# Performance work log

Hardware: AMD Instinct MI355X
Metric: run time of the kernel (lower is better)

Reference implementation:

```python
import jax, jax.numpy as jnp
import numpy as np
import math

B, T, D_MOTION = 2, 1536, 256
D_MODEL, N_HEADS, D_FF, N_LAYERS = 512, 8, 2048, 6
D_HEAD = D_MODEL // N_HEADS
FPS = 30
PERIOD = FPS // 2
CONTEXT_FRAMES = 10
NEG = -1e9  # large negative instead of -inf so fully-masked rows give uniform attn, not NaN


def _w(k, shape, fan_in):
    return jax.random.normal(k, shape, jnp.float32) / np.sqrt(fan_in)


def setup_inputs() -> dict:
    key = jax.random.key(0)
    ks = jax.random.split(key, 16)
    L = N_LAYERS
    din = D_MOTION + 5 + 1
    inp = {
        'motion': jax.random.normal(ks[0], (B, T, D_MOTION), jnp.float32),
        'traj': jax.random.normal(ks[1], (B, T, 5), jnp.float32),
        'me_w1': _w(ks[2], (din, D_MODEL), din), 'me_b1': jnp.zeros((D_MODEL,), jnp.float32),
        'me_w2': _w(ks[3], (D_MODEL, D_MODEL), D_MODEL), 'me_b2': jnp.zeros((D_MODEL,), jnp.float32),
        'wq': _w(ks[4], (L, D_MODEL, D_MODEL), D_MODEL), 'bq': jnp.zeros((L, D_MODEL), jnp.float32),
        'wk': _w(ks[5], (L, D_MODEL, D_MODEL), D_MODEL), 'bk': jnp.zeros((L, D_MODEL), jnp.float32),
        'wv': _w(ks[6], (L, D_MODEL, D_MODEL), D_MODEL), 'bv': jnp.zeros((L, D_MODEL), jnp.float32),
        'wo': _w(ks[7], (L, D_MODEL, D_MODEL), D_MODEL), 'bo': jnp.zeros((L, D_MODEL), jnp.float32),
        'ln1_g': jnp.ones((L, D_MODEL), jnp.float32), 'ln1_b': jnp.zeros((L, D_MODEL), jnp.float32),
        'ffn_w1': _w(ks[8], (L, D_MODEL, D_FF), D_MODEL), 'ffn_b1': jnp.zeros((L, D_FF), jnp.float32),
        'ffn_w2': _w(ks[9], (L, D_FF, D_MODEL), D_FF), 'ffn_b2': jnp.zeros((L, D_MODEL), jnp.float32),
        'ln2_g': jnp.ones((L, D_MODEL), jnp.float32), 'ln2_b': jnp.zeros((L, D_MODEL), jnp.float32),
        'fln_g': jnp.ones((D_MODEL,), jnp.float32), 'fln_b': jnp.zeros((D_MODEL,), jnp.float32),
        'dec_w1': _w(ks[10], (D_MODEL, D_MODEL), D_MODEL), 'dec_b1': jnp.zeros((D_MODEL,), jnp.float32),
        'dec_w2': _w(ks[11], (D_MODEL, D_MOTION), D_MODEL), 'dec_b2': jnp.zeros((D_MOTION,), jnp.float32),
    }
    return inp


def _layer_norm(x, g, b):
    m = jnp.mean(x, axis=-1, keepdims=True)
    v = jnp.mean((x - m) ** 2, axis=-1, keepdims=True)
    return (x - m) * jax.lax.rsqrt(v + 1e-5) * g + b


def _leaky(x):
    return jnp.where(x >= 0, x, 0.01 * x)


def _forward(motion, traj, me_w1, me_b1, me_w2, me_b2, wq, bq, wk, bk, wv, bv, wo, bo,
             ln1_g, ln1_b, ffn_w1, ffn_b1, ffn_w2, ffn_b2, ln2_g, ln2_b,
             fln_g, fln_b, dec_w1, dec_b1, dec_w2, dec_b2):
    idx = jnp.arange(T)
    dist = jnp.abs(idx[:, None] - idx[None, :])                       # [T,T]
    atten_bias = -(dist // PERIOD).astype(jnp.float32)                # periodic distance bias

    # context mask: keep first context_frames and last frame
    batch_mask = jnp.ones((T, 1), jnp.float32).at[CONTEXT_FRAMES:-1].set(0.0)
    mask = jnp.broadcast_to(batch_mask[None], (B, T, 1))              # [B,T,1]
    cf = jnp.ones((T,), bool).at[CONTEXT_FRAMES:-1].set(False)        # constrained frames

    original_motion = motion
    motion = motion * mask

    # motion encoder (dropout inactive at eval)
    h = jnp.concatenate([motion, traj, mask], axis=-1)                # [B,T,D_MOTION+6]
    x = _leaky(h @ me_w1 + me_b1)
    x = _leaky(x @ me_w2 + me_b2)

    # periodic positional embedding (sinusoidal on pos mod period)
    pos = jnp.mod(jnp.arange(T, dtype=jnp.float32), float(PERIOD))
    half = D_MODEL // 2
    div = jnp.exp(-np.log(10000.0) * (2.0 * jnp.arange(half, dtype=jnp.float32)) / D_MODEL)
    ang = pos[:, None] * div[None, :]
    pe = jnp.concatenate([jnp.sin(ang), jnp.cos(ang)], axis=-1)       # [T,D_MODEL]
    x = x + pe[None]

    # dynamically growing attention window
    num_trans = T - CONTEXT_FRAMES - 1
    ksz = math.ceil(num_trans / 2 / N_LAYERS) * 2 + 1
    kern = jnp.ones((ksz,), jnp.float32)
    thr = ksz // 2
    scale = 1.0 / np.sqrt(D_HEAD)

    for i in range(N_LAYERS):
        # attn mask: True = blocked
        amask = (dist > thr) | (~cf)[None, :]                         # [T,T]
        h = _layer_norm(x, ln1_g[i], ln1_b[i])                        # pre-layernorm
        q = (h @ wq[i] + bq[i]).reshape(B, T, N_HEADS, D_HEAD)
        k = (h @ wk[i] + bk[i]).reshape(B, T, N_HEADS, D_HEAD)
        v = (h @ wv[i] + bv[i]).reshape(B, T, N_HEADS, D_HEAD)
        scores = jnp.einsum('bqhd,bkhd->bhqk', q, k) * scale + atten_bias
        scores = jnp.where(amask[None, None], NEG, scores)
        attn = jax.nn.softmax(scores, axis=-1)
        out = jnp.einsum('bhqk,bkhd->bqhd', attn, v).reshape(B, T, D_MODEL)
        x = x + out @ wo[i] + bo[i]
        # position-wise FFN (pre-layernorm)
        h = _layer_norm(x, ln2_g[i], ln2_b[i])
        x = x + jax.nn.relu(h @ ffn_w1[i] + ffn_b1[i]) @ ffn_w2[i] + ffn_b2[i]
        # grow constrained frames by conv1d with ones kernel (same padding)
        cf = jnp.convolve(cf.astype(jnp.float32), kern, mode='same') > 0.5

    x = _layer_norm(x, fln_g, fln_b)
    x = _leaky(x @ dec_w1 + dec_b1)
    x = x @ dec_w2 + dec_b2                                           # [B,T,D_MOTION]
    out = original_motion * mask + x * (1.0 - mask)
    return out, mask


def reference(motion, traj, me_w1, me_b1, me_w2, me_b2, wq, bq, wk, bk, wv, bv, wo, bo,
              ln1_g, ln1_b, ffn_w1, ffn_b1, ffn_w2, ffn_b2, ln2_g, ln2_b,
              fln_g, fln_b, dec_w1, dec_b1, dec_w2, dec_b2):
    return _forward(motion, traj, me_w1, me_b1, me_w2, me_b2, wq, bq, wk, bk, wv, bv, wo, bo,
                    ln1_g, ln1_b, ffn_w1, ffn_b1, ffn_w2, ffn_b2, ln2_g, ln2_b,
                    fln_g, fln_b, dec_w1, dec_b1, dec_w2, dec_b2)
```

## Files before the change

kernel.cpp:

```cpp
#include <hip/hip_runtime.h>
#include <math.h>

typedef unsigned short ushort_t;
typedef unsigned int uint_t;
typedef __bf16 bf16x4 __attribute__((ext_vector_type(4)));
typedef __bf16 bf16x8 __attribute__((ext_vector_type(8)));
typedef float f32x4 __attribute__((ext_vector_type(4)));

#define T_SEQ   1536
#define NB      2
#define MROWS   3072
#define DMODEL  512
#define NHEADS  8
#define DHEAD   64
#define DFF     2048
#define DMOTION 256
#define NLAYERS 6
#define PERIODN 15
#define CTXF    10
#define THRW    128
#define KIN     384

__device__ __forceinline__ float bf2f(ushort_t u) { return __uint_as_float((uint_t)u << 16); }
__device__ __forceinline__ ushort_t f2bf(float f) {
    uint_t x = __float_as_uint(f);
    return (ushort_t)((x + 0x7fffu + ((x >> 16) & 1u)) >> 16);
}

__device__ __forceinline__ void gl2lds(const ushort_t* g, ushort_t* l) {
    __builtin_amdgcn_global_load_lds((const __attribute__((address_space(1))) void*)g,
                                     (__attribute__((address_space(3))) void*)l, 16, 0, 0);
}

__global__ __launch_bounds__(256) void pe_k(float* __restrict__ pe) {
    int idx = blockIdx.x * 256 + threadIdx.x;
    if (idx >= PERIODN * DMODEL) return;
    int p = idx / DMODEL, c = idx % DMODEL;
    int j = (c < DMODEL / 2) ? c : (c - DMODEL / 2);
    float div = __expf(-logf(10000.0f) * (2.0f * (float)j) / (float)DMODEL);
    float ang = (float)p * div;
    pe[idx] = (c < DMODEL / 2) ? sinf(ang) : cosf(ang);
}

__global__ __launch_bounds__(256) void build_k(const float* __restrict__ motion,
                                               const float* __restrict__ traj,
                                               ushort_t* __restrict__ hin,
                                               float* __restrict__ mask_out) {
    int idx = blockIdx.x * 256 + threadIdx.x;
    if (idx >= MROWS * KIN) return;
    int row = idx / KIN, c = idx % KIN;
    int t = row % T_SEQ;
    float mv = (t < CTXF || t == T_SEQ - 1) ? 1.0f : 0.0f;
    float val;
    if (c < DMOTION)            val = motion[(size_t)row * DMOTION + c] * mv;
    else if (c < DMOTION + 5)   val = traj[(size_t)row * 5 + (c - DMOTION)];
    else if (c == DMOTION + 5)  val = mv;
    else                        val = 0.0f;
    hin[idx] = f2bf(val);
    if (c == 0) mask_out[row] = mv;
}

__global__ __launch_bounds__(256)
void tconv_k(const float* __restrict__ src, size_t sstride,
             ushort_t* __restrict__ dst, size_t dstride,
             int K, int N, int Kpad) {
    __shared__ float t[32][33];
    src += (size_t)blockIdx.z * sstride;
    dst += (size_t)blockIdx.z * dstride;
    const int kb = blockIdx.y * 32, nb = blockIdx.x * 32;
    const int tx = threadIdx.x & 31, ty = threadIdx.x >> 5;
#pragma unroll
    for (int i = 0; i < 4; ++i) {
        int k = kb + ty + i * 8, n = nb + tx;
        t[ty + i * 8][tx] = (k < K && n < N) ? src[(size_t)k * N + n] : 0.0f;
    }
    __syncthreads();
#pragma unroll
    for (int i = 0; i < 4; ++i) {
        int n = nb + ty + i * 8, kk = kb + tx;
        if (n < N && kk < Kpad) dst[(size_t)n * Kpad + kk] = f2bf(t[tx][ty + i * 8]);
    }
}

__global__ __launch_bounds__(256)
void tconv_qkv_k(const float* __restrict__ wq, const float* __restrict__ wk,
                 const float* __restrict__ wv, ushort_t* __restrict__ qkvt) {
    __shared__ float t[32][33];
    const int z = blockIdx.z, s = z % 3, l = z / 3;
    const float* src = (s == 0 ? wq : s == 1 ? wk : wv) + (size_t)l * DMODEL * DMODEL;
    ushort_t* dst = qkvt + (size_t)z * DMODEL * DMODEL;
    const int kb = blockIdx.y * 32, nb = blockIdx.x * 32;
    const int tx = threadIdx.x & 31, ty = threadIdx.x >> 5;
#pragma unroll
    for (int i = 0; i < 4; ++i)
        t[ty + i * 8][tx] = src[(size_t)(kb + ty + i * 8) * DMODEL + nb + tx];
    __syncthreads();
#pragma unroll
    for (int i = 0; i < 4; ++i)
        dst[(size_t)(nb + ty + i * 8) * DMODEL + kb + tx] = f2bf(t[tx][ty + i * 8]);
}

__global__ __launch_bounds__(256)
void bcat_k(const float* __restrict__ bq, const float* __restrict__ bk,
            const float* __restrict__ bv, float* __restrict__ bqkv) {
    int idx = blockIdx.x * 256 + threadIdx.x;
    if (idx >= NLAYERS * 3 * DMODEL) return;
    int l = idx / (3 * DMODEL), n = idx % (3 * DMODEL);
    int s = n >> 9, c = n & 511;
    const float* b = (s == 0 ? bq : s == 1 ? bk : bv);
    bqkv[idx] = b[l * DMODEL + c];
}

#define CL  68
template <int ACT, bool RES, bool PE, bool OUTBF>
__global__ __launch_bounds__(256)
void qgemm_k(const ushort_t* __restrict__ A, int K,
             const ushort_t* __restrict__ Wt,
             const float* __restrict__ bias,
             const float* __restrict__ res,
             const float* __restrict__ pe15,
             void* __restrict__ Cout, int N) {
    __shared__ ushort_t smem[2][(32 + 64) * 128];
    const int tid = threadIdx.x;
    const int lane = tid & 63, wid = tid >> 6;
    const int m0 = blockIdx.y * 32, n0 = blockIdx.x * 64;
    const int l4 = lane >> 4, l15 = lane & 15;
    const int lrow = lane >> 4;
    const int lu   = lane & 15;

    f32x4 acc[2][4];
#pragma unroll
    for (int m = 0; m < 2; ++m)
#pragma unroll
        for (int n = 0; n < 4; ++n) acc[m][n] = (f32x4){0.f, 0.f, 0.f, 0.f};

    const int niter = K >> 7;

    auto stage = [&](int buf, int k0) {
        ushort_t* dst = &smem[buf][0];
#pragma unroll
        for (int j = 0; j < 6; ++j) {
            const int inst = wid * 6 + j;
            if (inst < 8) {
                const int row = inst * 4 + lrow;
                const int u = lu ^ (row & 15);
                gl2lds(A + (size_t)(m0 + row) * K + k0 + u * 8, dst + inst * 512);
            } else {
                const int bi = inst - 8;
                const int row = bi * 4 + lrow;
                const int u = lu ^ (row & 15);
                gl2lds(Wt + (size_t)(n0 + row) * K + k0 + u * 8,
                       dst + 32 * 128 + bi * 512);
            }
        }
    };

    const int kbyte = wid * 64;
    auto rdfrag = [&](const ushort_t* t, int row) -> bf16x8 {
        const int off0 = kbyte + l4 * 8;
        const int off1 = kbyte + 32 + l4 * 8;
        const int a0 = row * 256 + (((off0 & ~15) ^ ((row & 15) << 4)) | (off0 & 15));
        const int a1 = row * 256 + (((off1 & ~15) ^ ((row & 15) << 4)) | (off1 & 15));
        bf16x4 lo = *(const bf16x4*)((const char*)t + a0);
        bf16x4 hi = *(const bf16x4*)((const char*)t + a1);
        return __builtin_shufflevector(lo, hi, 0, 1, 2, 3, 4, 5, 6, 7);
    };

    stage(0, 0);
    __syncthreads();
    int cur = 0;
    for (int t = 0; t < niter; ++t) {
        if (t + 1 < niter) stage(cur ^ 1, (t + 1) << 7);
        const ushort_t* As = &smem[cur][0];
        const ushort_t* Bs = &smem[cur][32 * 128];
        bf16x8 af[2], bf[4];
#pragma unroll
        for (int m = 0; m < 2; ++m) af[m] = rdfrag(As, m * 16 + l15);
#pragma unroll
        for (int n = 0; n < 4; ++n) bf[n] = rdfrag(Bs, n * 16 + l15);
#pragma unroll
        for (int m = 0; m < 2; ++m)
#pragma unroll
            for (int n = 0; n < 4; ++n)
                acc[m][n] = __builtin_amdgcn_mfma_f32_16x16x32_bf16(af[m], bf[n], acc[m][n], 0, 0, 0);
        __syncthreads();
        cur ^= 1;
    }

    float* cb0 = (float*)&smem[0][0];
    float* cb1 = (float*)&smem[1][0];
    if (wid >= 2) {
        float* cb = (wid == 2) ? cb0 : cb1;
#pragma unroll
        for (int m = 0; m < 2; ++m)
#pragma unroll
            for (int n = 0; n < 4; ++n)
#pragma unroll
                for (int r = 0; r < 4; ++r)
                    cb[(m * 16 + l4 * 4 + r) * CL + n * 16 + l15] = acc[m][n][r];
    }
    __syncthreads();
    if (wid < 2) {
        float* cb = (wid == 0) ? cb0 : cb1;
#pragma unroll
        for (int m = 0; m < 2; ++m)
#pragma unroll
            for (int n = 0; n < 4; ++n)
#pragma unroll
                for (int r = 0; r < 4; ++r)
                    cb[(m * 16 + l4 * 4 + r) * CL + n * 16 + l15] += acc[m][n][r];
    }
    __syncthreads();

    const int row = tid >> 3, c0 = (tid & 7) * 8;
    const int grow = m0 + row;
#pragma unroll
    for (int j = 0; j < 8; ++j) {
        const int gcol = n0 + c0 + j;
        float v = cb0[row * CL + c0 + j] + cb1[row * CL + c0 + j] + bias[gcol];
        if (ACT == 1) v = v >= 0.f ? v : 0.01f * v;
        else if (ACT == 2) v = fmaxf(v, 0.f);
        else if (ACT == 3) {
            const int t2 = grow % T_SEQ;
            const float mv = (t2 < CTXF || t2 == T_SEQ - 1) ? 1.0f : 0.0f;
            v = res[(size_t)grow * N + gcol] * mv + v * (1.0f - mv);
        }
        if (PE) v += pe15[((grow % T_SEQ) % PERIODN) * DMODEL + gcol];
        if (RES) v += res[(size_t)grow * N + gcol];
        if (OUTBF) ((ushort_t*)Cout)[(size_t)grow * N + gcol] = f2bf(v);
        else       ((float*)Cout)[(size_t)grow * N + gcol] = v;
    }
}

__global__ __launch_bounds__(256)
void ln_k(const float* __restrict__ X, const float* __restrict__ g,
          const float* __restrict__ b, ushort_t* __restrict__ Y) {
    const int wid = threadIdx.x >> 6, lane = threadIdx.x & 63;
    const int row = blockIdx.x * 4 + wid;
    const float* x = X + (size_t)row * DMODEL;
    float v[8], s = 0.f;
#pragma unroll
    for (int j = 0; j < 8; ++j) { v[j] = x[lane + 64 * j]; s += v[j]; }
#pragma unroll
    for (int o = 32; o; o >>= 1) s += __shfl_xor(s, o);
    const float mean = s * (1.0f / DMODEL);
    float vs = 0.f;
#pragma unroll
    for (int j = 0; j < 8; ++j) { float d = v[j] - mean; vs += d * d; }
#pragma unroll
    for (int o = 32; o; o >>= 1) vs += __shfl_xor(vs, o);
    const float inv = rsqrtf(vs * (1.0f / DMODEL) + 1e-5f);
    ushort_t* y = Y + (size_t)row * DMODEL;
#pragma unroll
    for (int j = 0; j < 8; ++j) {
        const int c = lane + 64 * j;
        y[c] = f2bf((v[j] - mean) * inv * g[c] + b[c]);
    }
}

__global__ __launch_bounds__(1024)
void vsum_k(const ushort_t* __restrict__ h, float* __restrict__ hp) {
    __shared__ float red[1024];
    const int b = blockIdx.x, ch = blockIdx.y;
    const int c = threadIdx.x & 511, half = threadIdx.x >> 9;
    const ushort_t* hb = h + (size_t)(b * T_SEQ + ch * 192) * DMODEL + c;
    float s = 0.f;
    for (int r = half; r < 192; r += 2) s += bf2f(hb[(size_t)r * DMODEL]);
    red[threadIdx.x] = s;
    __syncthreads();
    if (threadIdx.x < 512)
        hp[(b * 8 + ch) * 512 + threadIdx.x] = red[threadIdx.x] + red[threadIdx.x + 512];
}

__global__ __launch_bounds__(256)
void vdot_k(const float* __restrict__ hp, const ushort_t* __restrict__ wvt,
            const float* __restrict__ bv, float* __restrict__ vm) {
    __shared__ float mh[512];
    __shared__ float red[256];
    const int b = blockIdx.x, seg = blockIdx.y;
    const int t = threadIdx.x;
    for (int c = t; c < 512; c += 256) {
        float s = 0.f;
#pragma unroll
        for (int ch = 0; ch < 8; ++ch) s += hp[(b * 8 + ch) * 512 + c];
        mh[c] = s * (1.0f / T_SEQ);
    }
    __syncthreads();
    const int col = seg * 128 + (t & 127);
    const int kh = (t >> 7) * 256;
    const ushort_t* w = wvt + (size_t)col * 512 + kh;
    float s = 0.f;
    for (int k = 0; k < 256; k += 8) {
        bf16x8 w8 = *(const bf16x8*)(w + k);
#pragma unroll
        for (int j = 0; j < 8; ++j) s += mh[kh + k + j] * (float)w8[j];
    }
    red[t] = s;
    __syncthreads();
    if (t < 128) vm[b * 512 + col] = red[t] + red[t + 128] + bv[col];
}

#define KLD 72
#define VLD 36
__global__ __launch_bounds__(256)
void attn3_k(const ushort_t* __restrict__ qkv, const float* __restrict__ vm,
             ushort_t* __restrict__ attout,
             int lo, int hi, int nlow, int qhi0, int tl, int st, int ft) {
    __shared__ ushort_t klds_[4][32 * KLD];
    __shared__ ushort_t vlds_[4][64 * VLD];
    const int lane = threadIdx.x & 63, wid = threadIdx.x >> 6;
    const int s = blockIdx.x * 4 + wid;
    const int h = blockIdx.y, b = blockIdx.z;
    if (s >= st) {
        const int f = s - st;
        if (f >= ft) return;
        const int r0 = nlow + 16 * f;
        const int rend = min(16, qhi0 - r0);
        const ushort_t ov = f2bf(vm[b * 512 + h * 64 + lane]);
        ushort_t* op = attout + (size_t)(b * T_SEQ + r0) * DMODEL + h * 64 + lane;
        for (int r = 0; r < rend; ++r) op[(size_t)r * DMODEL] = ov;
        return;
    }
    const int l15 = lane & 15, l4 = lane >> 4;

    int qb, qend;
    if (s < tl) { qb = 16 * s;                qend = nlow - 1; }
    else        { qb = qhi0 + 16 * (s - tl);  qend = T_SEQ - 1; }
    const int nr = qend - qb;

    ushort_t* klds = klds_[wid];
    ushort_t* vlds = vlds_[wid];
    const size_t rbase = (size_t)(b * T_SEQ) * 1536;
    const int q = qb + l15;

    const int qrow_r = min(q, T_SEQ - 1);
    const ushort_t* qptr = qkv + rbase + (size_t)qrow_r * 1536 + h * 64;
    bf16x8 bq[2];
#pragma unroll
    for (int kh = 0; kh < 2; ++kh) {
        bf16x4 lo4 = *(const bf16x4*)(qptr + kh * 32 + l4 * 4);
        bf16x4 hi4 = *(const bf16x4*)(qptr + kh * 32 + 16 + l4 * 4);
        bq[kh] = __builtin_shufflevector(lo4, hi4, 0, 1, 2, 3, 4, 5, 6, 7);
    }

    const int band0 = max(0, qb - THRW);
    const int band1 = min(T_SEQ - 1, qb + 15 + THRW);
    const int i1s = band0, i1e = min(band1, lo - 1);
    const int i2s = max(band0, hi), i2e = band1;

    f32x4 O[4] = {{0.f,0.f,0.f,0.f},{0.f,0.f,0.f,0.f},{0.f,0.f,0.f,0.f},{0.f,0.f,0.f,0.f}};
    float m = -3.0e38f, lsum = 0.f;

#pragma unroll 1
    for (int seg = 0; seg < 2; ++seg) {
        const int s0 = seg ? i2s : i1s, s1 = seg ? i2e : i1e;
#pragma unroll 1
        for (int c0 = s0; c0 <= s1; c0 += 32) {
#pragma unroll
            for (int i = 0; i < 4; ++i) {
                const int idx = i * 64 + lane;
                const int row = idx >> 3, c = (idx & 7) * 8;
                const int kr = min(c0 + row, T_SEQ - 1);
                const uint4 kv = *(const uint4*)(qkv + rbase + (size_t)kr * 1536 + 512 + h * 64 + c);
                *(uint4*)&klds[row * KLD + c] = kv;
                const uint4 vv = *(const uint4*)(qkv + rbase + (size_t)kr * 1536 + 1024 + h * 64 + c);
                const ushort_t* vp = (const ushort_t*)&vv;
#pragma unroll
                for (int d = 0; d < 8; ++d) vlds[(c + d) * VLD + row] = vp[d];
            }
            f32x4 sacc[2];
            __builtin_amdgcn_s_setprio(1);
#pragma unroll
            for (int ks = 0; ks < 2; ++ks) {
                f32x4 a = {0.f, 0.f, 0.f, 0.f};
#pragma unroll
                for (int kh = 0; kh < 2; ++kh) {
                    const ushort_t* kp = &klds[(16 * ks + l15) * KLD + kh * 32];
                    bf16x4 lo4 = *(const bf16x4*)(kp + l4 * 4);
                    bf16x4 hi4 = *(const bf16x4*)(kp + 16 + l4 * 4);
                    bf16x8 ak = __builtin_shufflevector(lo4, hi4, 0, 1, 2, 3, 4, 5, 6, 7);
                    a = __builtin_amdgcn_mfma_f32_16x16x32_bf16(ak, bq[kh], a, 0, 0, 0);
                }
                sacc[ks] = a;
            }
            __builtin_amdgcn_s_setprio(0);
            float sv[8];
            bool vld[8];
            float cm = -3.0e38f;
#pragma unroll
            for (int ks = 0; ks < 2; ++ks)
#pragma unroll
                for (int r = 0; r < 4; ++r) {
                    const int key = c0 + 16 * ks + 4 * l4 + r;
                    const int dist = (q > key) ? (q - key) : (key - q);
                    const bool v = (dist <= THRW) && (key < lo || key >= hi) && (key < T_SEQ);
                    const int ii = ks * 4 + r;
                    sv[ii] = sacc[ks][r] * 0.125f - (float)(dist / PERIODN);
                    vld[ii] = v;
                    cm = fmaxf(cm, v ? sv[ii] : -3.0e38f);
                }
            cm = fmaxf(cm, __shfl_xor(cm, 16));
            cm = fmaxf(cm, __shfl_xor(cm, 32));
            const float mnew = fmaxf(m, cm);
            const float sc = __expf(m - mnew);
            m = mnew;
            float p[8], psum = 0.f;
#pragma unroll
            for (int ii = 0; ii < 8; ++ii) {
                p[ii] = vld[ii] ? __expf(sv[ii] - mnew) : 0.f;
                psum += p[ii];
            }
            psum += __shfl_xor(psum, 16);
            psum += __shfl_xor(psum, 32);
            lsum = lsum * sc + psum;
#pragma unroll
            for (int ds = 0; ds < 4; ++ds) O[ds] *= sc;
            bf16x8 pb;
#pragma unroll
            for (int ii = 0; ii < 8; ++ii) pb[ii] = (__bf16)p[ii];
            __builtin_amdgcn_s_setprio(1);
#pragma unroll
            for (int ds = 0; ds < 4; ++ds) {
                const ushort_t* vp2 = &vlds[(16 * ds + l15) * VLD];
                bf16x4 lo4 = *(const bf16x4*)(vp2 + 4 * l4);
                bf16x4 hi4 = *(const bf16x4*)(vp2 + 16 + 4 * l4);
                bf16x8 av = __builtin_shufflevector(lo4, hi4, 0, 1, 2, 3, 4, 5, 6, 7);
                O[ds] = __builtin_amdgcn_mfma_f32_16x16x32_bf16(av, pb, O[ds], 0, 0, 0);
            }
            __builtin_amdgcn_s_setprio(0);
        }
    }
    if (l15 <= nr) {
        const float inv = 1.0f / lsum;
        ushort_t* op = attout + (size_t)(b * T_SEQ + qb + l15) * DMODEL + h * 64;
#pragma unroll
        for (int ds = 0; ds < 4; ++ds)
#pragma unroll
            for (int r = 0; r < 4; ++r)
                op[16 * ds + 4 * l4 + r] = f2bf(O[ds][r] * inv);
    }
}

extern "C" void kernel_launch(void* const* d_in, const int* in_sizes, int n_in,
                              void* d_out, int out_size, void* d_ws, size_t ws_size,
                              hipStream_t stream) {
    const float* motion = (const float*)d_in[0];
    const float* traj   = (const float*)d_in[1];
    const float* me_w1  = (const float*)d_in[2];
    const float* me_b1  = (const float*)d_in[3];
    const float* me_w2  = (const float*)d_in[4];
    const float* me_b2  = (const float*)d_in[5];
    const float* wq = (const float*)d_in[6];
    const float* bq = (const float*)d_in[7];
    const float* wk = (const float*)d_in[8];
    const float* bk = (const float*)d_in[9];
    const float* wv = (const float*)d_in[10];
    const float* bv = (const float*)d_in[11];
    const float* wo = (const float*)d_in[12];
    const float* bo = (const float*)d_in[13];
    const float* ln1_g = (const float*)d_in[14];
    const float* ln1_b = (const float*)d_in[15];
    const float* ffn_w1 = (const float*)d_in[16];
    const float* ffn_b1 = (const float*)d_in[17];
    const float* ffn_w2 = (const float*)d_in[18];
    const float* ffn_b2 = (const float*)d_in[19];
    const float* ln2_g = (const float*)d_in[20];
    const float* ln2_b = (const float*)d_in[21];
    const float* fln_g = (const float*)d_in[22];
    const float* fln_b = (const float*)d_in[23];
    const float* dec_w1 = (const float*)d_in[24];
    const float* dec_b1 = (const float*)d_in[25];
    const float* dec_w2 = (const float*)d_in[26];
    const float* dec_b2 = (const float*)d_in[27];

    float* out = (float*)d_out;
    float* mask_out = out + (size_t)MROWS * DMOTION;

    char* base = (char*)d_ws;
    auto alloc = [&](size_t bytes) { char* p = base; base += (bytes + 255) & ~(size_t)255; return p; };

    ushort_t* qkvt  = (ushort_t*)alloc((size_t)NLAYERS * 1536 * 512 * 2);
    ushort_t* wot   = (ushort_t*)alloc((size_t)NLAYERS * 512 * 512 * 2);
    ushort_t* ffn1t = (ushort_t*)alloc((size_t)NLAYERS * 2048 * 512 * 2);
    ushort_t* ffn2t = (ushort_t*)alloc((size_t)NLAYERS * 512 * 2048 * 2);
    ushort_t* mew1t = (ushort_t*)alloc((size_t)512 * KIN * 2);
    ushort_t* mew2t = (ushort_t*)alloc((size_t)512 * 512 * 2);
    ushort_t* dec1t = (ushort_t*)alloc((size_t)512 * 512 * 2);
    ushort_t* dec2t = (ushort_t*)alloc((size_t)256 * 512 * 2);
    float*    bqkv  = (float*)alloc((size_t)NLAYERS * 1536 * 4);
    float*    pe15  = (float*)alloc((size_t)PERIODN * DMODEL * 4);
    float*    hp    = (float*)alloc((size_t)NB * 8 * 512 * 4);
    float*    vm    = (float*)alloc((size_t)NB * 512 * 4);
    ushort_t* hin   = (ushort_t*)alloc((size_t)MROWS * KIN * 2);
    float*    x     = (float*)alloc((size_t)MROWS * DMODEL * 4);
    ushort_t* h     = (ushort_t*)alloc((size_t)MROWS * DMODEL * 2);
    ushort_t* qkv   = (ushort_t*)alloc((size_t)MROWS * 1536 * 2);
    ushort_t* ff    = (ushort_t*)alloc((size_t)MROWS * DFF * 2);

    const dim3 blk(256);
    pe_k<<<(PERIODN * DMODEL + 255) / 256, blk, 0, stream>>>(pe15);
    build_k<<<(MROWS * KIN + 255) / 256, blk, 0, stream>>>(motion, traj, hin, mask_out);

    tconv_qkv_k<<<dim3(16, 16, 18), blk, 0, stream>>>(wq, wk, wv, qkvt);
    tconv_k<<<dim3(16, 16, 6), blk, 0, stream>>>(wo, 512 * 512, wot, 512 * 512, 512, 512, 512);
    tconv_k<<<dim3(64, 16, 6), blk, 0, stream>>>(ffn_w1, 512 * 2048, ffn1t, 2048 * 512, 512, 2048, 512);
    tconv_k<<<dim3(16, 64, 6), blk, 0, stream>>>(ffn_w2, 2048 * 512, ffn2t, 512 * 2048, 2048, 512, 2048);
    tconv_k<<<dim3(16, 12, 1), blk, 0, stream>>>(me_w1, 0, mew1t, 0, 262, 512, KIN);
    tconv_k<<<dim3(16, 16, 1), blk, 0, stream>>>(me_w2, 0, mew2t, 0, 512, 512, 512);
    tconv_k<<<dim3(16, 16, 1), blk, 0, stream>>>(dec_w1, 0, dec1t, 0, 512, 512, 512);
    tconv_k<<<dim3(8, 16, 1),  blk, 0, stream>>>(dec_w2, 0, dec2t, 0, 512, 256, 512);
    bcat_k<<<(NLAYERS * 1536 + 255) / 256, blk, 0, stream>>>(bq, bk, bv, bqkv);

    const dim3 gs512(8, 96), gs1536(24, 96), gsff(32, 96), gs256(4, 96);

    qgemm_k<1, false, false, true ><<<gs512, blk, 0, stream>>>(hin, KIN, mew1t, me_b1, nullptr, nullptr, h, 512);
    qgemm_k<1, false, true,  false><<<gs512, blk, 0, stream>>>(h, 512, mew2t, me_b2, nullptr, pe15, x, 512);

    for (int i = 0; i < NLAYERS; ++i) {
        const int lo = CTXF + THRW * i;
        const int hi = (T_SEQ - 1) - THRW * i;
        int qlow_end = lo + 127;
        int qhi0 = hi - 128;
        int nlow, ninact;
        if (qhi0 <= qlow_end + 1) {
            nlow = T_SEQ; qhi0 = T_SEQ; ninact = 0;
        } else {
            nlow = qlow_end + 1;
            ninact = qhi0 - nlow;
        }
        const int tl2 = (nlow + 15) / 16;
        const int th2 = (T_SEQ - qhi0 + 15) / 16;
        const int st  = tl2 + th2;
        const int ft  = (ninact + 15) / 16;

        ln_k<<<MROWS / 4, blk, 0, stream>>>(x, ln1_g + i * 512, ln1_b + i * 512, h);
        qgemm_k<0, false, false, true><<<gs1536, blk, 0, stream>>>(h, 512, qkvt + (size_t)i * 1536 * 512, bqkv + i * 1536, nullptr, nullptr, qkv, 1536);
        if (ninact > 0) {
            vsum_k<<<dim3(NB, 8), dim3(1024), 0, stream>>>(h, hp);
            vdot_k<<<dim3(NB, 4), blk, 0, stream>>>(hp, qkvt + (size_t)i * 1536 * 512 + (size_t)1024 * 512, bqkv + i * 1536 + 1024, vm);
        }
        attn3_k<<<dim3((st + ft + 3) / 4, NHEADS, NB), blk, 0, stream>>>(qkv, vm, h, lo, hi, nlow, qhi0, tl2, st, ft);
        qgemm_k<0, true, false, false><<<gs512, blk, 0, stream>>>(h, 512, wot + (size_t)i * 512 * 512, bo + i * 512, x, nullptr, x, 512);
        ln_k<<<MROWS / 4, blk, 0, stream>>>(x, ln2_g + i * 512, ln2_b + i * 512, h);
        qgemm_k<2, false, false, true><<<gsff, blk, 0, stream>>>(h, 512, ffn1t + (size_t)i * 2048 * 512, ffn_b1 + i * 2048, nullptr, nullptr, ff, 2048);
        qgemm_k<0, true, false, false><<<gs512, blk, 0, stream>>>(ff, 2048, ffn2t + (size_t)i * 512 * 2048, ffn_b2 + i * 512, x, nullptr, x, 512);
    }

    ln_k<<<MROWS / 4, blk, 0, stream>>>(x, fln_g, fln_b, h);
    qgemm_k<1, false, false, true ><<<gs512, blk, 0, stream>>>(h, 512, dec1t, dec_b1, nullptr, nullptr, ff, 512);
    qgemm_k<3, false, false, false><<<gs256, blk, 0, stream>>>(ff, 512, dec2t, dec_b2, motion, nullptr, out, 256);
}
```

Baseline: 851.9 us.

## Compute Q/K/V and output projections only for active query and key rows

Replaces the full-sequence QKV GEMM with row-gathered GEMMs. Q is computed only for active query rows and K/V only for unmasked key rows. The output projection is likewise restricted to active rows. For fully masked query rows, the uniform-attention result is folded algebraically: the mean V vector is passed through Wo by a small GEMV and added to the residual directly. It also vectorises vsum and removes the setprio hints in attention. This cuts GEMM work in later layers, where the active band is small, at the cost of extra small launches.

Result: faster. 831.2 us (-2.4%).

```diff
diff --git a/kernel.cpp b/kernel.cpp
--- a/kernel.cpp
+++ b/kernel.cpp
@@ -232,6 +232,129 @@
     }
 }
 
+template <bool RES, bool OUTBF>
+__global__ __launch_bounds__(256)
+void pgemm_k(const ushort_t* __restrict__ A,
+             const ushort_t* __restrict__ Wt,
+             const float* __restrict__ bias,
+             const float* __restrict__ res,
+             void* __restrict__ Cout, int ldc,
+             int tpb, int len1, int start2, int nact) {
+    __shared__ ushort_t smem[2][(32 + 64) * 128];
+    const int tid = threadIdx.x;
+    const int lane = tid & 63, wid = tid >> 6;
+    const int ty = blockIdx.y;
+    const int bb = (ty >= tpb) ? 1 : 0;
+    const int t32 = (ty - bb * tpb) * 32;
+    const int n0 = blockIdx.x * 64;
+    const int l4 = lane >> 4, l15 = lane & 15;
+    const int lrow = lane >> 4;
+    const int lu   = lane & 15;
+
+    auto maprow = [&](int pr) -> size_t {
+        int r = t32 + pr;
+        r = min(r, nact - 1);
+        int tt = (r < len1) ? r : (start2 + (r - len1));
+        return (size_t)(bb * T_SEQ + tt);
+    };
+
+    f32x4 acc[2][4];
+#pragma unroll
+    for (int m = 0; m < 2; ++m)
+#pragma unroll
+        for (int n = 0; n < 4; ++n) acc[m][n] = (f32x4){0.f, 0.f, 0.f, 0.f};
+
+    auto stage = [&](int buf, int k0) {
+        ushort_t* dst = &smem[buf][0];
+#pragma unroll
+        for (int j = 0; j < 6; ++j) {
+            const int inst = wid * 6 + j;
+            if (inst < 8) {
+                const int row = inst * 4 + lrow;
+                const int u = lu ^ (row & 15);
+                gl2lds(A + maprow(row) * 512 + k0 + u * 8, dst + inst * 512);
+            } else {
+                const int bi = inst - 8;
+                const int row = bi * 4 + lrow;
+                const int u = lu ^ (row & 15);
+                gl2lds(Wt + (size_t)(n0 + row) * 512 + k0 + u * 8,
+                       dst + 32 * 128 + bi * 512);
+            }
+        }
+    };
+
+    const int kbyte = wid * 64;
+    auto rdfrag = [&](const ushort_t* t, int row) -> bf16x8 {
+        const int off0 = kbyte + l4 * 8;
+        const int off1 = kbyte + 32 + l4 * 8;
+        const int a0 = row * 256 + (((off0 & ~15) ^ ((row & 15) << 4)) | (off0 & 15));
+        const int a1 = row * 256 + (((off1 & ~15) ^ ((row & 15) << 4)) | (off1 & 15));
+        bf16x4 lo = *(const bf16x4*)((const char*)t + a0);
+        bf16x4 hi = *(const bf16x4*)((const char*)t + a1);
+        return __builtin_shufflevector(lo, hi, 0, 1, 2, 3, 4, 5, 6, 7);
+    };
+
+    stage(0, 0);
+    __syncthreads();
+    int cur = 0;
+    for (int t = 0; t < 4; ++t) {
+        if (t + 1 < 4) stage(cur ^ 1, (t + 1) << 7);
+        const ushort_t* As = &smem[cur][0];
+        const ushort_t* Bs = &smem[cur][32 * 128];
+        bf16x8 af[2], bf[4];
+#pragma unroll
+        for (int m = 0; m < 2; ++m) af[m] = rdfrag(As, m * 16 + l15);
+#pragma unroll
+        for (int n = 0; n < 4; ++n) bf[n] = rdfrag(Bs, n * 16 + l15);
+#pragma unroll
+        for (int m = 0; m < 2; ++m)
+#pragma unroll
+            for (int n = 0; n < 4; ++n)
+                acc[m][n] = __builtin_amdgcn_mfma_f32_16x16x32_bf16(af[m], bf[n], acc[m][n], 0, 0, 0);
+        __syncthreads();
+        cur ^= 1;
+    }
+
+    float* cb0 = (float*)&smem[0][0];
+    float* cb1 = (float*)&smem[1][0];
+    if (wid >= 2) {
+        float* cb = (wid == 2) ? cb0 : cb1;
+#pragma unroll
+        for (int m = 0; m < 2; ++m)
+#pragma unroll
+            for (int n = 0; n < 4; ++n)
+#pragma unroll
+                for (int r = 0; r < 4; ++r)
+                    cb[(m * 16 + l4 * 4 + r) * CL + n * 16 + l15] = acc[m][n][r];
+    }
+    __syncthreads();
+    if (wid < 2) {
+        float* cb = (wid == 0) ? cb0 : cb1;
+#pragma unroll
+        for (int m = 0; m < 2; ++m)
+#pragma unroll
+            for (int n = 0; n < 4; ++n)
+#pragma unroll
+                for (int r = 0; r < 4; ++r)
+                    cb[(m * 16 + l4 * 4 + r) * CL + n * 16 + l15] += acc[m][n][r];
+    }
+    __syncthreads();
+
+    const int row = tid >> 3, c0 = (tid & 7) * 8;
+    const int pr = t32 + row;
+    if (pr >= nact) return;
+    const int tt = (pr < len1) ? pr : (start2 + (pr - len1));
+    const size_t grow = (size_t)(bb * T_SEQ + tt);
+#pragma unroll
+    for (int j = 0; j < 8; ++j) {
+        const int gcol = n0 + c0 + j;
+        float v = cb0[row * CL + c0 + j] + cb1[row * CL + c0 + j] + bias[gcol];
+        if (RES) v += res[grow * ldc + gcol];
+        if (OUTBF) ((ushort_t*)Cout)[grow * ldc + gcol] = f2bf(v);
+        else       ((float*)Cout)[grow * ldc + gcol] = v;
+    }
+}
+
 __global__ __launch_bounds__(256)
 void ln_k(const float* __restrict__ X, const float* __restrict__ g,
           const float* __restrict__ b, ushort_t* __restrict__ Y) {
@@ -260,16 +383,26 @@
 
 __global__ __launch_bounds__(1024)
 void vsum_k(const ushort_t* __restrict__ h, float* __restrict__ hp) {
-    __shared__ float red[1024];
+    __shared__ float red[16][512];
     const int b = blockIdx.x, ch = blockIdx.y;
-    const int c = threadIdx.x & 511, half = threadIdx.x >> 9;
-    const ushort_t* hb = h + (size_t)(b * T_SEQ + ch * 192) * DMODEL + c;
-    float s = 0.f;
-    for (int r = half; r < 192; r += 2) s += bf2f(hb[(size_t)r * DMODEL]);
-    red[threadIdx.x] = s;
-    __syncthreads();
-    if (threadIdx.x < 512)
-        hp[(b * 8 + ch) * 512 + threadIdx.x] = red[threadIdx.x] + red[threadIdx.x + 512];
+    const int rg = threadIdx.x >> 6;
+    const int c8 = (threadIdx.x & 63) * 8;
+    const ushort_t* hb = h + (size_t)(b * T_SEQ + ch * 192) * DMODEL + c8;
+    float a[8] = {};
+    for (int r = rg; r < 192; r += 16) {
+        bf16x8 v = *(const bf16x8*)(hb + (size_t)r * DMODEL);
+#pragma unroll
+        for (int j = 0; j < 8; ++j) a[j] += (float)v[j];
+    }
+#pragma unroll
+    for (int j = 0; j < 8; ++j) red[rg][c8 + j] = a[j];
+    __syncthreads();
+    if (threadIdx.x < 512) {
+        float s = 0.f;
+#pragma unroll
+        for (int gi = 0; gi < 16; ++gi) s += red[gi][threadIdx.x];
+        hp[(b * 8 + ch) * 512 + threadIdx.x] = s;
+    }
 }
 
 __global__ __launch_bounds__(256)
@@ -300,27 +433,49 @@
     if (t < 128) vm[b * 512 + col] = red[t] + red[t + 128] + bv[col];
 }
 
+__global__ __launch_bounds__(256)
+void gemv_k(const float* __restrict__ vin, const ushort_t* __restrict__ wt,
+            const float* __restrict__ bias, float* __restrict__ vout) {
+    __shared__ float mh[512];
+    __shared__ float red[256];
+    const int b = blockIdx.x, seg = blockIdx.y;
+    const int t = threadIdx.x;
+    for (int c = t; c < 512; c += 256) mh[c] = vin[b * 512 + c];
+    __syncthreads();
+    const int col = seg * 128 + (t & 127);
+    const int kh = (t >> 7) * 256;
+    const ushort_t* w = wt + (size_t)col * 512 + kh;
+    float s = 0.f;
+    for (int k = 0; k < 256; k += 8) {
+        bf16x8 w8 = *(const bf16x8*)(w + k);
+#pragma unroll
+        for (int j = 0; j < 8; ++j) s += mh[kh + k + j] * (float)w8[j];
+    }
+    red[t] = s;
+    __syncthreads();
+    if (t < 128) vout[b * 512 + col] = red[t] + red[t + 128] + bias[col];
+}
+
+__global__ __launch_bounds__(256)
+void xadd_k(const float* __restrict__ vmo, float* __restrict__ x, int q0) {
+    const int row = q0 + blockIdx.x, b = blockIdx.y;
+    float* xr = x + (size_t)(b * T_SEQ + row) * DMODEL;
+    const float* vb = vmo + b * 512;
+    xr[threadIdx.x]       += vb[threadIdx.x];
+    xr[threadIdx.x + 256] += vb[threadIdx.x + 256];
+}
+
 #define KLD 72
 #define VLD 36
 __global__ __launch_bounds__(256)
-void attn3_k(const ushort_t* __restrict__ qkv, const float* __restrict__ vm,
-             ushort_t* __restrict__ attout,
-             int lo, int hi, int nlow, int qhi0, int tl, int st, int ft) {
+void attn3_k(const ushort_t* __restrict__ qkv, ushort_t* __restrict__ attout,
+             int lo, int hi, int nlow, int qhi0, int tl, int st) {
     __shared__ ushort_t klds_[4][32 * KLD];
     __shared__ ushort_t vlds_[4][64 * VLD];
     const int lane = threadIdx.x & 63, wid = threadIdx.x >> 6;
     const int s = blockIdx.x * 4 + wid;
+    if (s >= st) return;
     const int h = blockIdx.y, b = blockIdx.z;
-    if (s >= st) {
-        const int f = s - st;
-        if (f >= ft) return;
-        const int r0 = nlow + 16 * f;
-        const int rend = min(16, qhi0 - r0);
-        const ushort_t ov = f2bf(vm[b * 512 + h * 64 + lane]);
-        ushort_t* op = attout + (size_t)(b * T_SEQ + r0) * DMODEL + h * 64 + lane;
-        for (int r = 0; r < rend; ++r) op[(size_t)r * DMODEL] = ov;
-        return;
-    }
     const int l15 = lane & 15, l4 = lane >> 4;
 
     int qb, qend;
@@ -369,7 +524,6 @@
                 for (int d = 0; d < 8; ++d) vlds[(c + d) * VLD + row] = vp[d];
             }
             f32x4 sacc[2];
-            __builtin_amdgcn_s_setprio(1);
 #pragma unroll
             for (int ks = 0; ks < 2; ++ks) {
                 f32x4 a = {0.f, 0.f, 0.f, 0.f};
@@ -383,7 +537,6 @@
                 }
                 sacc[ks] = a;
             }
-            __builtin_amdgcn_s_setprio(0);
             float sv[8];
             bool vld[8];
             float cm = -3.0e38f;
@@ -418,7 +571,6 @@
             bf16x8 pb;
 #pragma unroll
             for (int ii = 0; ii < 8; ++ii) pb[ii] = (__bf16)p[ii];
-            __builtin_amdgcn_s_setprio(1);
 #pragma unroll
             for (int ds = 0; ds < 4; ++ds) {
                 const ushort_t* vp2 = &vlds[(16 * ds + l15) * VLD];
@@ -427,7 +579,6 @@
                 bf16x8 av = __builtin_shufflevector(lo4, hi4, 0, 1, 2, 3, 4, 5, 6, 7);
                 O[ds] = __builtin_amdgcn_mfma_f32_16x16x32_bf16(av, pb, O[ds], 0, 0, 0);
             }
-            __builtin_amdgcn_s_setprio(0);
         }
     }
     if (l15 <= nr) {
@@ -491,6 +642,7 @@
     float*    pe15  = (float*)alloc((size_t)PERIODN * DMODEL * 4);
     float*    hp    = (float*)alloc((size_t)NB * 8 * 512 * 4);
     float*    vm    = (float*)alloc((size_t)NB * 512 * 4);
+    float*    vmo   = (float*)alloc((size_t)NB * 512 * 4);
     ushort_t* hin   = (ushort_t*)alloc((size_t)MROWS * KIN * 2);
     float*    x     = (float*)alloc((size_t)MROWS * DMODEL * 4);
     ushort_t* h     = (ushort_t*)alloc((size_t)MROWS * DMODEL * 2);
@@ -511,7 +663,7 @@
     tconv_k<<<dim3(8, 16, 1),  blk, 0, stream>>>(dec_w2, 0, dec2t, 0, 512, 256, 512);
     bcat_k<<<(NLAYERS * 1536 + 255) / 256, blk, 0, stream>>>(bq, bk, bv, bqkv);
 
-    const dim3 gs512(8, 96), gs1536(24, 96), gsff(32, 96), gs256(4, 96);
+    const dim3 gs512(8, 96), gsff(32, 96), gs256(4, 96);
 
     qgemm_k<1, false, false, true ><<<gs512, blk, 0, stream>>>(hin, KIN, mew1t, me_b1, nullptr, nullptr, h, 512);
     qgemm_k<1, false, true,  false><<<gs512, blk, 0, stream>>>(h, 512, mew2t, me_b2, nullptr, pe15, x, 512);
@@ -531,16 +683,30 @@
         const int tl2 = (nlow + 15) / 16;
         const int th2 = (T_SEQ - qhi0 + 15) / 16;
         const int st  = tl2 + th2;
-        const int ft  = (ninact + 15) / 16;
+        const int nact_q = nlow + (T_SEQ - qhi0);
+        const int tpb_q  = (nact_q + 31) / 32;
+        const int nkeys  = lo + (T_SEQ - hi);
+        const int tpb_kv = (nkeys + 31) / 32;
+
+        const ushort_t* qw  = qkvt + (size_t)i * 1536 * 512;
+        const ushort_t* kvw = qw + (size_t)512 * 512;
+        const ushort_t* vw  = qw + (size_t)1024 * 512;
+        const float* bq_i   = bqkv + i * 1536;
 
         ln_k<<<MROWS / 4, blk, 0, stream>>>(x, ln1_g + i * 512, ln1_b + i * 512, h);
-        qgemm_k<0, false, false, true><<<gs1536, blk, 0, stream>>>(h, 512, qkvt + (size_t)i * 1536 * 512, bqkv + i * 1536, nullptr, nullptr, qkv, 1536);
+        pgemm_k<false, true><<<dim3(8, 2 * tpb_q), blk, 0, stream>>>(
+            h, qw, bq_i, nullptr, qkv, 1536, tpb_q, nlow, qhi0, nact_q);
+        pgemm_k<false, true><<<dim3(16, 2 * tpb_kv), blk, 0, stream>>>(
+            h, kvw, bq_i + 512, nullptr, qkv + 512, 1536, tpb_kv, lo, hi, nkeys);
         if (ninact > 0) {
             vsum_k<<<dim3(NB, 8), dim3(1024), 0, stream>>>(h, hp);
-            vdot_k<<<dim3(NB, 4), blk, 0, stream>>>(hp, qkvt + (size_t)i * 1536 * 512 + (size_t)1024 * 512, bqkv + i * 1536 + 1024, vm);
+            vdot_k<<<dim3(NB, 4), blk, 0, stream>>>(hp, vw, bq_i + 1024, vm);
+            gemv_k<<<dim3(NB, 4), blk, 0, stream>>>(vm, wot + (size_t)i * 512 * 512, bo + i * 512, vmo);
+            xadd_k<<<dim3(ninact, NB), blk, 0, stream>>>(vmo, x, nlow);
         }
-        attn3_k<<<dim3((st + ft + 3) / 4, NHEADS, NB), blk, 0, stream>>>(qkv, vm, h, lo, hi, nlow, qhi0, tl2, st, ft);
-        qgemm_k<0, true, false, false><<<gs512, blk, 0, stream>>>(h, 512, wot + (size_t)i * 512 * 512, bo + i * 512, x, nullptr, x, 512);
+        attn3_k<<<dim3((st + 3) / 4, NHEADS, NB), blk, 0, stream>>>(qkv, h, lo, hi, nlow, qhi0, tl2, st);
+        pgemm_k<true, false><<<dim3(8, 2 * tpb_q), blk, 0, stream>>>(
+            h, wot + (size_t)i * 512 * 512, bo + i * 512, x, x, 512, tpb_q, nlow, qhi0, nact_q);
         ln_k<<<MROWS / 4, blk, 0, stream>>>(x, ln2_g + i * 512, ln2_b + i * 512, h);
         qgemm_k<2, false, false, true><<<gsff, blk, 0, stream>>>(h, 512, ffn1t + (size_t)i * 2048 * 512, ffn_b1 + i * 2048, nullptr, nullptr, ff, 2048);
         qgemm_k<0, true, false, false><<<gs512, blk, 0, stream>>>(ff, 2048, ffn2t + (size_t)i * 512 * 2048, ffn_b2 + i * 512, x, nullptr, x, 512);
```
